# Kernel optimization log

Measured on AMD Instinct MI355X. Metric: run time of the kernel, lower is better.

## Reference

```python
import jax, jax.numpy as jnp
import numpy as np

# dims
B, NN, D, HD, L, H, S, FIN = 2048, 64, 128, 128, 4, 8, 8, 16
N = B * NN              # total nodes = 131072
EPG = 8 * NN            # edges per graph (avg degree 8)
E = B * EPG             # total edges = 1048576
A = S * (S - 1)         # num_actions per head = 56


def setup_inputs() -> dict:
    key = jax.random.key(0)
    ks = jax.random.split(key, 16)
    def nrm(k, shape, scale=0.05):
        return jax.random.normal(k, shape, jnp.float32) * scale
    x = jax.random.normal(ks[0], (N, FIN), jnp.float32)
    # per-graph random edges (src/dst local in [0, NN), offset by graph id)
    off = jnp.repeat(jnp.arange(B, dtype=jnp.int32) * NN, EPG)
    src = jax.random.randint(ks[1], (E,), 0, NN, jnp.int32) + off
    dst = jax.random.randint(ks[2], (E,), 0, NN, jnp.int32) + off
    edge_index = jnp.stack([src, dst])
    batch = (jnp.arange(N, dtype=jnp.int32) // NN)
    subsets = jnp.arange(H * S, dtype=jnp.int32).reshape(H, S)
    return dict(
        x=x, edge_index=edge_index, batch=batch, subsets=subsets,
        W_in=nrm(ks[3], (FIN, D)), b_in=jnp.zeros(D, jnp.float32),
        W_self=nrm(ks[4], (L, D, D)), W_nbr=nrm(ks[5], (L, D, D)),
        b_enc=jnp.zeros((L, D), jnp.float32),
        ext_W=nrm(ks[6], (H, 2 * D, HD)), ext_b=jnp.zeros((H, HD), jnp.float32),
        ln_g=jnp.ones((H, HD), jnp.float32), ln_b=jnp.zeros((H, HD), jnp.float32),
        hub_W=nrm(ks[7], (HD, HD)), hub_b=jnp.zeros(HD, jnp.float32),
        pol_W1=nrm(ks[8], (H, 2 * HD, HD)), pol_b1=jnp.zeros((H, HD), jnp.float32),
        pol_W2=nrm(ks[9], (H, HD, A)), pol_b2=jnp.zeros((H, A), jnp.float32),
        val_W1=nrm(ks[10], (D, D)), val_b1=jnp.zeros(D, jnp.float32),
        val_W2=nrm(ks[11], (D, 1)), val_b2=jnp.zeros(1, jnp.float32),
    )


def _forward(floats, edge_index, batch, subsets):
    (x, W_in, b_in, W_self, W_nbr, b_enc, ext_W, ext_b, ln_g, ln_b,
     hub_W, hub_b, pol_W1, pol_b1, pol_W2, pol_b2,
     val_W1, val_b1, val_W2, val_b2) = floats
    src, dst = edge_index[0], edge_index[1]
    # --- GraphEncoder: input proj + L layers of mean-aggregate message passing ---
    deg = jnp.maximum(
        jax.ops.segment_sum(jnp.ones(src.shape[0], x.dtype), dst, num_segments=N), 1.0
    )[:, None]
    h = jax.nn.relu(x @ W_in + b_in)                      # [N, D]
    for l in range(L):
        agg = jax.ops.segment_sum(h[src], dst, num_segments=N) / deg
        h = jax.nn.relu(h @ W_self[l] + agg @ W_nbr[l] + b_enc[l])
    # --- batched per-graph / per-head subset pooling (replaces python loop) ---
    he = h.reshape(B, NN, D)                              # graphs are contiguous in `batch`
    sub = he[:, subsets]                                  # [B, H, S, D]
    pooled = jnp.concatenate([sub.mean(2), sub.max(2)], axis=-1)   # [B, H, 2D]
    z = jnp.einsum('bhf,hfd->bhd', pooled, ext_W) + ext_b
    mu = z.mean(-1, keepdims=True)
    var = z.var(-1, keepdims=True)
    head_emb = jax.nn.relu((z - mu) / jnp.sqrt(var + 1e-5) * ln_g + ln_b)  # [B, H, HD]
    # --- CommunicationHub: shared global context from mean over heads ---
    ctx = jax.nn.relu(head_emb.mean(1) @ hub_W + hub_b)   # [B, HD]
    # --- PolicyHeads: per-head MLP on concat(head_emb, context) ---
    pc = jnp.concatenate(
        [head_emb, jnp.broadcast_to(ctx[:, None, :], head_emb.shape)], axis=-1)
    hh = jax.nn.relu(jnp.einsum('bhf,hfd->bhd', pc, pol_W1) + pol_b1)
    logits = jnp.einsum('bhd,hda->bha', hh, pol_W2) + pol_b2       # [B, H, A]
    # --- ValueHead: per-graph mean pool -> MLP -> tanh ---
    gm = he.mean(1)                                        # segment mean (equal-size graphs)
    v = jnp.tanh(jax.nn.relu(gm @ val_W1 + val_b1) @ val_W2 + val_b2)  # [B, 1]
    return logits, v


def reference(x, edge_index, batch, subsets, W_in, b_in, W_self, W_nbr, b_enc,
              ext_W, ext_b, ln_g, ln_b, hub_W, hub_b, pol_W1, pol_b1, pol_W2,
              pol_b2, val_W1, val_b1, val_W2, val_b2):
    floats = (x, W_in, b_in, W_self, W_nbr, b_enc, ext_W, ext_b, ln_g, ln_b,
              hub_W, hub_b, pol_W1, pol_b1, pol_W2, pol_b2,
              val_W1, val_b1, val_W2, val_b2)
    return _forward(floats, edge_index, batch, subsets)
```

## Files before the change

kernel.cpp:

```cpp
#include <hip/hip_runtime.h>

#define E_TOT 1048576
#define LOGITS 917504

typedef short bf16x8 __attribute__((ext_vector_type(8)));
typedef float f32x4 __attribute__((ext_vector_type(4)));
typedef unsigned short u16;
typedef unsigned int u32;

#define DEV static __device__ __forceinline__

DEV u16 f2bf(float f){ u32 u = __float_as_uint(f); return (u16)((u + 0x7fffu + ((u>>16)&1u))>>16); }
DEV u32 pack2(float a, float b){ return (u32)f2bf(a) | ((u32)f2bf(b)<<16); }
DEV float bf2f(u16 h){ return __uint_as_float(((u32)h)<<16); }
DEV void unpack8(uint4 u, float* f){
  f[0]=__uint_as_float(u.x<<16); f[1]=__uint_as_float(u.x&0xffff0000u);
  f[2]=__uint_as_float(u.y<<16); f[3]=__uint_as_float(u.y&0xffff0000u);
  f[4]=__uint_as_float(u.z<<16); f[5]=__uint_as_float(u.z&0xffff0000u);
  f[6]=__uint_as_float(u.w<<16); f[7]=__uint_as_float(u.w&0xffff0000u);
}
DEV uint4 pack8(const float* f){
  uint4 u; u.x=pack2(f[0],f[1]); u.y=pack2(f[2],f[3]); u.z=pack2(f[4],f[5]); u.w=pack2(f[6],f[7]); return u;
}

#define GNN_E   0
#define EXT_E   131072
#define POL1_E  393216
#define POL2_E  655360
#define HUB_E   720896
#define VW1T_E  737280
#define POOL_E  753664
#define CTX_E   4947968

__global__ __launch_bounds__(256) void pack_w(
    const float* __restrict__ Wself, const float* __restrict__ Wnbr,
    const float* __restrict__ extW,  const float* __restrict__ polW1,
    const float* __restrict__ polW2, const float* __restrict__ hubW,
    const float* __restrict__ valW1, const float* __restrict__ W_in,
    u16* __restrict__ ws)
{
  int idx = (blockIdx.x*256 + threadIdx.x)<<3;
  float v[8];
  if (idx < 131072){
    int l = idx>>15, r = idx&32767;
    int m = (r>>14)&1, r2 = r&16383;
    int kb=(r2>>12)&3, ct=(r2>>9)&7, lane=(r2>>3)&63;
    int k0 = kb*32 + ((lane>>4)<<3), n = (ct<<4)+(lane&15);
    const float* W = m? Wnbr : Wself;
    #pragma unroll
    for (int j=0;j<8;j++) v[j]=W[(l<<14)+((k0+j)<<7)+n];
    *(uint4*)&ws[GNN_E+idx]=pack8(v);
  } else if (idx < 655360){
    int i = idx - 131072;
    int isPol = (i >= 262144); if (isPol) i -= 262144;
    int h = i>>15, r = i&32767;
    int kb=(r>>12)&7, ct=(r>>9)&7, lane=(r>>3)&63;
    int k0 = kb*32 + ((lane>>4)<<3), n = (ct<<4)+(lane&15);
    const float* W = isPol? polW1 : extW;
    #pragma unroll
    for (int j=0;j<8;j++) v[j]=W[(h<<15)+((k0+j)<<7)+n];
    *(uint4*)&ws[(isPol?POL1_E:EXT_E)+i]=pack8(v);
  } else if (idx < 720896){
    int i = idx - 655360;
    int h = i>>13, r = i&8191;
    int kb=(r>>11)&3, ct=(r>>9)&3, lane=(r>>3)&63;
    int k0=kb*32+((lane>>4)<<3), n=(ct<<4)+(lane&15);
    #pragma unroll
    for (int j=0;j<8;j++) v[j]=(n<56)? polW2[h*7168+(k0+j)*56+n] : 0.0f;
    *(uint4*)&ws[POL2_E+i]=pack8(v);
  } else if (idx < 737280){
    int i = idx-720896;
    int kb=(i>>12)&3, ct=(i>>9)&7, lane=(i>>3)&63;
    int k0=kb*32+((lane>>4)<<3), n=(ct<<4)+(lane&15);
    #pragma unroll
    for (int j=0;j<8;j++) v[j]=hubW[((k0+j)<<7)+n];
    *(uint4*)&ws[HUB_E+i]=pack8(v);
  } else if (idx < 753664){
    int i = idx-737280;
    int c = i>>7, k0 = i&127;
    #pragma unroll
    for (int j=0;j<8;j++) v[j]=valW1[((k0+j)<<7)+c];
    *(uint4*)&ws[VW1T_E+i]=pack8(v);
  } else if (idx < 757760){
    int i = idx-753664;
    int ct=(i>>9)&7, lane=(i>>3)&63;
    int k0=((lane>>4)<<3), n=(ct<<4)+(lane&15);
    #pragma unroll
    for (int j=0;j<8;j++) v[j]=(k0+j<16)? W_in[((k0+j)<<7)+n] : 0.0f;
    *(uint4*)&ws[CTX_E+i]=pack8(v);
  }
}

DEV void epi_write(u16* h_bf, u16* ht, f32x4 (&acc)[4][2], float b0, float b1,
                   int wv, int r15, int kh)
{
  float bias[2] = {b0, b1};
  #pragma unroll
  for (int rt=0;rt<4;rt++){
    int sch = (rt<<1)+(kh>>1);
    int r0  = (rt<<4)+(kh<<2);
    #pragma unroll
    for (int cc=0;cc<2;cc++){
      int col=(wv<<5)+(cc<<4)+r15;
      float v0=fmaxf(acc[rt][cc][0]+bias[cc],0.0f);
      float v1=fmaxf(acc[rt][cc][1]+bias[cc],0.0f);
      float v2=fmaxf(acc[rt][cc][2]+bias[cc],0.0f);
      float v3=fmaxf(acc[rt][cc][3]+bias[cc],0.0f);
      int chc=(col>>3);
      h_bf[((r0+0)<<7)+(((chc^((r0+0)&7))<<3)|(col&7))]=f2bf(v0);
      h_bf[((r0+1)<<7)+(((chc^((r0+1)&7))<<3)|(col&7))]=f2bf(v1);
      h_bf[((r0+2)<<7)+(((chc^((r0+2)&7))<<3)|(col&7))]=f2bf(v2);
      h_bf[((r0+3)<<7)+(((chc^((r0+3)&7))<<3)|(col&7))]=f2bf(v3);
      uint2 w; w.x=pack2(v0,v1); w.y=pack2(v2,v3);
      *(uint2*)&ht[(col<<6)+(((sch^(col&7))<<3)|((kh&1)<<2))]=w;
    }
  }
}

__global__ __launch_bounds__(256,3) void gnn_kernel(
  const float* __restrict__ x, const int* __restrict__ ei,
  const int* __restrict__ subsets, const float* __restrict__ b_in,
  const float* __restrict__ b_enc, const float* __restrict__ val_b1,
  const float* __restrict__ val_W2, const float* __restrict__ val_b2,
  const u16* __restrict__ packGNN, const u16* __restrict__ packWIN,
  const u16* __restrict__ valW1T,
  u16* __restrict__ pooled, float* __restrict__ out)
{
  __shared__ __align__(16) u16 h_bf[8192];
  __shared__ __align__(16) u16 ht[8192];
  __shared__ __align__(16) u16 agg_bf[8192];
  __shared__ float deg_inv[64];
  __shared__ int subs_s[64];
  __shared__ float gmbuf[128];
  __shared__ float redbuf[4];

  int t=threadIdx.x, b=blockIdx.x;
  int lane=t&63, wv=t>>6, r15=lane&15, kh=lane>>4, ctb=wv<<1;
  u32* cnt=(u32*)ht;
  f32x4 zero4={0.0f,0.0f,0.0f,0.0f};

  int e0=(b<<9)+(t<<1);
  int2 sp=*(const int2*)&ei[e0];
  int2 dp=*(const int2*)&ei[E_TOT+e0];
  int s0=sp.x&63, s1=sp.y&63, d0=dp.x&63, d1=dp.y&63;
  if (t<64) subs_s[t]=subsets[t];
  for (int i=t;i<1024;i+=256) ((uint4*)cnt)[i]=make_uint4(0,0,0,0);
  __syncthreads();
  atomicAdd(&cnt[(d0<<6)+((((s0>>3)^(d0&7))<<3)|(s0&7))],1u);
  atomicAdd(&cnt[(d1<<6)+((((s1>>3)^(d1&7))<<3)|(s1&7))],1u);
  __syncthreads();
  if (t<64){
    u32 s=0;
    for (int k2=0;k2<16;k2++){ uint4 vv=((uint4*)cnt)[(t<<4)+k2]; s+=vv.x+vv.y+vv.z+vv.w; }
    deg_inv[t]=1.0f/(float)(s>0u?s:1u);
  }
  __syncthreads();

  bf16x8 adjf[4][2];
  #pragma unroll
  for (int ct=0;ct<4;ct++){
    int dst=(ct<<4)+r15; float di=deg_inv[dst];
    #pragma unroll
    for (int kb=0;kb<2;kb++){
      int cb=(kb<<2)+kh;
      const u32* p=&cnt[(dst<<6)+((cb^(dst&7))<<3)];
      uint4 lo=*(const uint4*)p, hi=*(const uint4*)(p+4);
      uint4 pk;
      pk.x=pack2((float)lo.x*di,(float)lo.y*di);
      pk.y=pack2((float)lo.z*di,(float)lo.w*di);
      pk.z=pack2((float)hi.x*di,(float)hi.y*di);
      pk.w=pack2((float)hi.z*di,(float)hi.w*di);
      adjf[ct][kb]=*(bf16x8*)&pk;
    }
  }

  u16* xb=agg_bf;
  { int row=t>>2, c0=(t&3)<<3;
    float v[8];
    if (c0<16){
      const float* xg=x+(b<<10)+(row<<4)+c0;
      #pragma unroll
      for (int j=0;j<8;j++) v[j]=xg[j];
    } else {
      #pragma unroll
      for (int j=0;j<8;j++) v[j]=0.0f;
    }
    *(uint4*)&xb[(row<<5)+((((c0>>3)^(row&3))<<3))]=pack8(v);
  }
  __syncthreads();

  {
    bf16x8 bw0=*(const bf16x8*)&packWIN[(ctb<<9)+(lane<<3)];
    bf16x8 bw1=*(const bf16x8*)&packWIN[((ctb+1)<<9)+(lane<<3)];
    f32x4 acc[4][2];
    #pragma unroll
    for (int rt=0;rt<4;rt++){ acc[rt][0]=zero4; acc[rt][1]=zero4; }
    #pragma unroll
    for (int rt=0;rt<4;rt++){
      int row=(rt<<4)+r15;
      bf16x8 af=*(const bf16x8*)&xb[(row<<5)+((kh^(row&3))<<3)];
      acc[rt][0]=__builtin_amdgcn_mfma_f32_16x16x32_bf16(af,bw0,acc[rt][0],0,0,0);
      acc[rt][1]=__builtin_amdgcn_mfma_f32_16x16x32_bf16(af,bw1,acc[rt][1],0,0,0);
    }
    float bi0=b_in[(wv<<5)+r15], bi1=b_in[(wv<<5)+16+r15];
    epi_write(h_bf,ht,acc,bi0,bi1,wv,r15,kh);
  }
  __syncthreads();

  #pragma unroll 1
  for (int l=0;l<4;l++){
    const u16* pl = packGNN + (l<<15);
    f32x4 a2[2][4];
    #pragma unroll
    for (int rt=0;rt<2;rt++){ a2[rt][0]=zero4; a2[rt][1]=zero4; a2[rt][2]=zero4; a2[rt][3]=zero4; }
    #pragma unroll
    for (int kb=0;kb<2;kb++){
      #pragma unroll
      for (int rt=0;rt<2;rt++){
        int dim=((ctb+rt)<<4)+r15;
        bf16x8 af=*(const bf16x8*)&ht[(dim<<6)+((((kb<<2)+kh)^(dim&7))<<3)];
        #pragma unroll
        for (int ct=0;ct<4;ct++)
          a2[rt][ct]=__builtin_amdgcn_mfma_f32_16x16x32_bf16(af,adjf[ct][kb],a2[rt][ct],0,0,0);
      }
    }
    #pragma unroll
    for (int rt=0;rt<2;rt++){
      int dch=((ctb+rt)<<1)+(kh>>1);
      #pragma unroll
      for (int ct=0;ct<4;ct++){
        int node=(ct<<4)+r15;
        uint2 w; w.x=pack2(a2[rt][ct][0],a2[rt][ct][1]); w.y=pack2(a2[rt][ct][2],a2[rt][ct][3]);
        *(uint2*)&agg_bf[(node<<7)+(((dch^(node&7))<<3)|((kh&1)<<2))]=w;
      }
    }
    __syncthreads();
    f32x4 acc[4][2];
    #pragma unroll
    for (int rt=0;rt<4;rt++){ acc[rt][0]=zero4; acc[rt][1]=zero4; }
    #pragma unroll 2
    for (int kb=0;kb<4;kb++){
      int ch=(kb<<2)+kh;
      bf16x8 bs0=*(const bf16x8*)&pl[(kb<<12)+(ctb<<9)+(lane<<3)];
      bf16x8 bs1=*(const bf16x8*)&pl[(kb<<12)+((ctb+1)<<9)+(lane<<3)];
      bf16x8 bn0=*(const bf16x8*)&pl[16384+(kb<<12)+(ctb<<9)+(lane<<3)];
      bf16x8 bn1=*(const bf16x8*)&pl[16384+(kb<<12)+((ctb+1)<<9)+(lane<<3)];
      #pragma unroll
      for (int rt=0;rt<4;rt++){
        int row=(rt<<4)+r15;
        bf16x8 af=*(const bf16x8*)&h_bf[(row<<7)+((ch^(row&7))<<3)];
        acc[rt][0]=__builtin_amdgcn_mfma_f32_16x16x32_bf16(af,bs0,acc[rt][0],0,0,0);
        acc[rt][1]=__builtin_amdgcn_mfma_f32_16x16x32_bf16(af,bs1,acc[rt][1],0,0,0);
      }
      #pragma unroll
      for (int rt=0;rt<4;rt++){
        int row=(rt<<4)+r15;
        bf16x8 ag=*(const bf16x8*)&agg_bf[(row<<7)+((ch^(row&7))<<3)];
        acc[rt][0]=__builtin_amdgcn_mfma_f32_16x16x32_bf16(ag,bn0,acc[rt][0],0,0,0);
        acc[rt][1]=__builtin_amdgcn_mfma_f32_16x16x32_bf16(ag,bn1,acc[rt][1],0,0,0);
      }
    }
    float be0=b_enc[(l<<7)+(wv<<5)+r15], be1=b_enc[(l<<7)+(wv<<5)+16+r15];
    __syncthreads();
    epi_write(h_bf,ht,acc,be0,be1,wv,r15,kh);
    __syncthreads();
  }

  {
    int hd=t>>5, q=t&31, cb=q<<2;
    float ms[4]={0,0,0,0}, mx[4]={-3e38f,-3e38f,-3e38f,-3e38f};
    int ch=cb>>3;
    #pragma unroll
    for (int s=0;s<8;s++){
      int row=subs_s[(hd<<3)+s]; int sw=row&7;
      uint2 u=*(const uint2*)&h_bf[(row<<7)+(((ch^sw)<<3)|(cb&7))];
      float f0=__uint_as_float(u.x<<16), f1=__uint_as_float(u.x&0xffff0000u);
      float f2=__uint_as_float(u.y<<16), f3=__uint_as_float(u.y&0xffff0000u);
      ms[0]+=f0; ms[1]+=f1; ms[2]+=f2; ms[3]+=f3;
      mx[0]=fmaxf(mx[0],f0); mx[1]=fmaxf(mx[1],f1);
      mx[2]=fmaxf(mx[2],f2); mx[3]=fmaxf(mx[3],f3);
    }
    int base=(((b<<3)+hd)<<8);
    uint2 um,ux;
    um.x=pack2(ms[0]*0.125f,ms[1]*0.125f); um.y=pack2(ms[2]*0.125f,ms[3]*0.125f);
    ux.x=pack2(mx[0],mx[1]);               ux.y=pack2(mx[2],mx[3]);
    *(uint2*)&pooled[base+cb]    =um;
    *(uint2*)&pooled[base+128+cb]=ux;
  }

  float gsum=0.0f;
  if (t<128){
    #pragma unroll
    for (int c=0;c<8;c++){
      uint4 u=*(const uint4*)&ht[(t<<6)+(c<<3)];
      float f[8]; unpack8(u,f);
      gsum+=f[0]+f[1]+f[2]+f[3]+f[4]+f[5]+f[6]+f[7];
    }
  }
  __syncthreads();
  if (t<128) gmbuf[t]=gsum*0.015625f;
  __syncthreads();
  if (t<128){
    float acc=val_b1[t];
    const uint4* wr=(const uint4*)&valW1T[t<<7];
    #pragma unroll
    for (int c=0;c<16;c++){
      uint4 u=wr[c]; float f[8]; unpack8(u,f);
      const float* gp=&gmbuf[c<<3];
      #pragma unroll
      for (int j=0;j<8;j++) acc=fmaf(gp[j],f[j],acc);
    }
    float contrib=fmaxf(acc,0.0f)*val_W2[t];
    #pragma unroll
    for (int d=1;d<64;d<<=1) contrib+=__shfl_xor(contrib,d);
    if (lane==0) redbuf[wv]=contrib;
  }
  __syncthreads();
  if (t==0) out[LOGITS+b]=tanhf(redbuf[0]+redbuf[1]+val_b2[0]);
}

__global__ __launch_bounds__(256) void head1_kernel(
  u16* __restrict__ pooled, const u16* __restrict__ packExt,
  const float* __restrict__ ext_b, const float* __restrict__ ln_g,
  const float* __restrict__ ln_b)
{
  __shared__ __align__(16) u16 A_lds[4096];
  __shared__ float zf[16*132];
  int t=threadIdx.x, gb=blockIdx.x, hd=blockIdx.y;
  int lane=t&63, wv=t>>6, r15=lane&15, kh=lane>>4, ctb=wv<<1;
  for (int i=t;i<512;i+=256){
    int row=i>>5, ch=i&31;
    uint4 u=*(const uint4*)&pooled[(((((gb<<4)+row)<<3)+hd)<<8)+(ch<<3)];
    *(uint4*)&A_lds[(row<<8)+((ch^(row&7))<<3)]=u;
  }
  __syncthreads();
  const u16* pw=packExt+(hd<<15);
  bf16x8 bw[8][2];
  #pragma unroll
  for (int kb=0;kb<8;kb++){
    bw[kb][0]=*(const bf16x8*)&pw[(kb<<12)+(ctb<<9)+(lane<<3)];
    bw[kb][1]=*(const bf16x8*)&pw[(kb<<12)+((ctb+1)<<9)+(lane<<3)];
  }
  f32x4 zero4={0.0f,0.0f,0.0f,0.0f};
  f32x4 acc[2]={zero4,zero4};
  #pragma unroll
  for (int kb=0;kb<8;kb++){
    int ch=(kb<<2)+kh;
    bf16x8 a=*(const bf16x8*)&A_lds[(r15<<8)+((ch^(r15&7))<<3)];
    acc[0]=__builtin_amdgcn_mfma_f32_16x16x32_bf16(a,bw[kb][0],acc[0],0,0,0);
    acc[1]=__builtin_amdgcn_mfma_f32_16x16x32_bf16(a,bw[kb][1],acc[1],0,0,0);
  }
  float eb[2]={ext_b[(hd<<7)+(wv<<5)+r15], ext_b[(hd<<7)+(wv<<5)+16+r15]};
  #pragma unroll
  for (int cc=0;cc<2;cc++){
    int col=(wv<<5)+(cc<<4)+r15;
    #pragma unroll
    for (int i=0;i<4;i++) zf[((kh<<2)+i)*132+col]=acc[cc][i]+eb[cc];
  }
  __syncthreads();
  int row=t>>4, q=t&15;
  const float* zr=&zf[row*132+(q<<3)];
  float s=0,ss=0;
  #pragma unroll
  for (int i=0;i<8;i++){ float v=zr[i]; s+=v; ss+=v*v; }
  s+=__shfl_xor(s,1); ss+=__shfl_xor(ss,1);
  s+=__shfl_xor(s,2); ss+=__shfl_xor(ss,2);
  s+=__shfl_xor(s,4); ss+=__shfl_xor(ss,4);
  s+=__shfl_xor(s,8); ss+=__shfl_xor(ss,8);
  float mu=s*0.0078125f, var=ss*0.0078125f-mu*mu, rstd=rsqrtf(var+1e-5f);
  const float* g=&ln_g[(hd<<7)+(q<<3)];
  const float* bb=&ln_b[(hd<<7)+(q<<3)];
  float e[8];
  #pragma unroll
  for (int i=0;i<8;i++) e[i]=fmaxf((zr[i]-mu)*rstd*g[i]+bb[i],0.0f);
  *(uint4*)&pooled[(((((gb<<4)+row)<<3)+hd)<<8)+(q<<3)]=pack8(e);
}

__global__ __launch_bounds__(256) void ctx_kernel(
  const u16* __restrict__ pooled, const u16* __restrict__ packHub,
  const float* __restrict__ hub_b, u16* __restrict__ ctx)
{
  __shared__ __align__(16) u16 m_lds[2048];
  int t=threadIdx.x, gb=blockIdx.x;
  int lane=t&63, wv=t>>6, r15=lane&15, kh=lane>>4, ctb=wv<<1;
  {
    int row=t>>4, ch=t&15;
    float a8[8]={0,0,0,0,0,0,0,0};
    #pragma unroll
    for (int h=0;h<8;h++){
      uint4 u=*(const uint4*)&pooled[(((((gb<<4)+row)<<3)+h)<<8)+(ch<<3)];
      float f[8]; unpack8(u,f);
      #pragma unroll
      for (int k=0;k<8;k++) a8[k]+=f[k];
    }
    #pragma unroll
    for (int k=0;k<8;k++) a8[k]*=0.125f;
    *(uint4*)&m_lds[(row<<7)+((ch^(row&7))<<3)]=pack8(a8);
  }
  __syncthreads();
  bf16x8 bh[4][2];
  #pragma unroll
  for (int kb=0;kb<4;kb++){
    bh[kb][0]=*(const bf16x8*)&packHub[(kb<<12)+(ctb<<9)+(lane<<3)];
    bh[kb][1]=*(const bf16x8*)&packHub[(kb<<12)+((ctb+1)<<9)+(lane<<3)];
  }
  f32x4 zero4={0.0f,0.0f,0.0f,0.0f};
  f32x4 acc[2]={zero4,zero4};
  #pragma unroll
  for (int kb=0;kb<4;kb++){
    int ch=(kb<<2)+kh;
    bf16x8 a=*(const bf16x8*)&m_lds[(r15<<7)+((ch^(r15&7))<<3)];
    acc[0]=__builtin_amdgcn_mfma_f32_16x16x32_bf16(a,bh[kb][0],acc[0],0,0,0);
    acc[1]=__builtin_amdgcn_mfma_f32_16x16x32_bf16(a,bh[kb][1],acc[1],0,0,0);
  }
  float hb[2]={hub_b[(wv<<5)+r15], hub_b[(wv<<5)+16+r15]};
  #pragma unroll
  for (int cc=0;cc<2;cc++){
    int col=(wv<<5)+(cc<<4)+r15;
    #pragma unroll
    for (int i=0;i<4;i++){
      int row=(kh<<2)+i;
      ctx[(((gb<<4)+row)<<7)+col]=f2bf(fmaxf(acc[cc][i]+hb[cc],0.0f));
    }
  }
}

__global__ __launch_bounds__(256) void pol_kernel(
  const u16* __restrict__ pooled, const u16* __restrict__ ctx,
  const u16* __restrict__ packPol1, const u16* __restrict__ packPol2,
  const float* __restrict__ pol_b1, const float* __restrict__ pol_b2,
  float* __restrict__ out)
{
  __shared__ __align__(16) u16 A_lds[4096];
  __shared__ __align__(16) u16 hh[2048];
  int t=threadIdx.x, gb=blockIdx.x, hd=blockIdx.y;
  int lane=t&63, wv=t>>6, r15=lane&15, kh=lane>>4, ctb=wv<<1;
  for (int i=t;i<512;i+=256){
    int row=i>>5, ch=i&31;
    uint4 u;
    if (ch<16) u=*(const uint4*)&pooled[(((((gb<<4)+row)<<3)+hd)<<8)+(ch<<3)];
    else       u=*(const uint4*)&ctx[(((gb<<4)+row)<<7)+((ch-16)<<3)];
    *(uint4*)&A_lds[(row<<8)+((ch^(row&7))<<3)]=u;
  }
  __syncthreads();
  const u16* pw=packPol1+(hd<<15);
  bf16x8 bw[8][2];
  #pragma unroll
  for (int kb=0;kb<8;kb++){
    bw[kb][0]=*(const bf16x8*)&pw[(kb<<12)+(ctb<<9)+(lane<<3)];
    bw[kb][1]=*(const bf16x8*)&pw[(kb<<12)+((ctb+1)<<9)+(lane<<3)];
  }
  f32x4 zero4={0.0f,0.0f,0.0f,0.0f};
  f32x4 acc[2]={zero4,zero4};
  #pragma unroll
  for (int kb=0;kb<8;kb++){
    int ch=(kb<<2)+kh;
    bf16x8 a=*(const bf16x8*)&A_lds[(r15<<8)+((ch^(r15&7))<<3)];
    acc[0]=__builtin_amdgcn_mfma_f32_16x16x32_bf16(a,bw[kb][0],acc[0],0,0,0);
    acc[1]=__builtin_amdgcn_mfma_f32_16x16x32_bf16(a,bw[kb][1],acc[1],0,0,0);
  }
  float pb[2]={pol_b1[(hd<<7)+(wv<<5)+r15], pol_b1[(hd<<7)+(wv<<5)+16+r15]};
  #pragma unroll
  for (int cc=0;cc<2;cc++){
    int col=(wv<<5)+(cc<<4)+r15;
    #pragma unroll
    for (int i=0;i<4;i++){
      int row=(kh<<2)+i;
      float v=fmaxf(acc[cc][i]+pb[cc],0.0f);
      hh[(row<<7)+((((col>>3)^(row&7))<<3)|(col&7))]=f2bf(v);
    }
  }
  __syncthreads();
  const u16* p2=packPol2+(hd<<13);
  bf16x8 b2[4];
  #pragma unroll
  for (int kb=0;kb<4;kb++)
    b2[kb]=*(const bf16x8*)&p2[(kb<<11)+(wv<<9)+(lane<<3)];
  f32x4 a2=zero4;
  #pragma unroll
  for (int kb=0;kb<4;kb++){
    int ch=(kb<<2)+kh;
    bf16x8 a=*(const bf16x8*)&hh[(r15<<7)+((ch^(r15&7))<<3)];
    a2=__builtin_amdgcn_mfma_f32_16x16x32_bf16(a,b2[kb],a2,0,0,0);
  }
  int col=(wv<<4)+r15;
  if (col<56){
    float pb2=pol_b2[hd*56+col];
    #pragma unroll
    for (int i=0;i<4;i++){
      int row=(kh<<2)+i;
      out[(((((gb<<4)+row)<<3)+hd)*56)+col]=a2[i]+pb2;
    }
  }
}

extern "C" void kernel_launch(void* const* d_in, const int* in_sizes, int n_in,
                              void* d_out, int out_size, void* d_ws, size_t ws_size,
                              hipStream_t stream)
{
  const float* x     =(const float*)d_in[0];
  const int*   ei    =(const int*)  d_in[1];
  const int*   subs  =(const int*)  d_in[3];
  const float* W_in  =(const float*)d_in[4];
  const float* b_in  =(const float*)d_in[5];
  const float* W_self=(const float*)d_in[6];
  const float* W_nbr =(const float*)d_in[7];
  const float* b_enc =(const float*)d_in[8];
  const float* extW  =(const float*)d_in[9];
  const float* ext_b =(const float*)d_in[10];
  const float* ln_g  =(const float*)d_in[11];
  const float* ln_b  =(const float*)d_in[12];
  const float* hubW  =(const float*)d_in[13];
  const float* hub_b =(const float*)d_in[14];
  const float* polW1 =(const float*)d_in[15];
  const float* pol_b1=(const float*)d_in[16];
  const float* polW2 =(const float*)d_in[17];
  const float* pol_b2=(const float*)d_in[18];
  const float* valW1 =(const float*)d_in[19];
  const float* val_b1=(const float*)d_in[20];
  const float* valW2 =(const float*)d_in[21];
  const float* val_b2=(const float*)d_in[22];
  float* out=(float*)d_out;
  u16* ws=(u16*)d_ws;

  pack_w<<<370,256,0,stream>>>(W_self,W_nbr,extW,polW1,polW2,hubW,valW1,W_in,ws);
  gnn_kernel<<<2048,256,0,stream>>>(x,ei,subs,b_in,b_enc,val_b1,valW2,val_b2,
      ws+GNN_E, ws+CTX_E, ws+VW1T_E, ws+POOL_E, out);
  head1_kernel<<<dim3(128,8),256,0,stream>>>(ws+POOL_E, ws+EXT_E, ext_b, ln_g, ln_b);
  ctx_kernel<<<128,256,0,stream>>>(ws+POOL_E, ws+HUB_E, hub_b, ws+CTX_E);
  pol_kernel<<<dim3(128,8),256,0,stream>>>(ws+POOL_E, ws+CTX_E, ws+POL1_E, ws+POL2_E,
      pol_b1, pol_b2, out);
}
```

Baseline: 192.3 us.

## Fuse extractor, hub and policy head kernels into one per-graph-block kernel

Merges the three head kernels (extractor+LayerNorm, communication hub, policy MLP) into a single kernel where each block handles 8 graphs and loops over all 8 heads. Intermediate head embeddings and context stay in LDS instead of round-tripping through global memory, and two kernel launches are dropped. The cost is a smaller grid (256 blocks instead of 1024) and half-empty MFMA tiles, since only 8 of 16 rows are valid. Head loops are also serialized, with extra barriers per head.

```diff
diff --git a/kernel.cpp b/kernel.cpp
--- a/kernel.cpp
+++ b/kernel.cpp
@@ -319,76 +319,80 @@
   if (t==0) out[LOGITS+b]=tanhf(redbuf[0]+redbuf[1]+val_b2[0]);
 }
 
-__global__ __launch_bounds__(256) void head1_kernel(
-  u16* __restrict__ pooled, const u16* __restrict__ packExt,
+__global__ __launch_bounds__(256) void heads_kernel(
+  const u16* __restrict__ pooled, const u16* __restrict__ packExt,
   const float* __restrict__ ext_b, const float* __restrict__ ln_g,
-  const float* __restrict__ ln_b)
+  const float* __restrict__ ln_b, const u16* __restrict__ packHub,
+  const float* __restrict__ hub_b, const u16* __restrict__ packPol1,
+  const u16* __restrict__ packPol2, const float* __restrict__ pol_b1,
+  const float* __restrict__ pol_b2, float* __restrict__ out)
 {
-  __shared__ __align__(16) u16 A_lds[4096];
-  __shared__ float zf[16*132];
-  int t=threadIdx.x, gb=blockIdx.x, hd=blockIdx.y;
-  int lane=t&63, wv=t>>6, r15=lane&15, kh=lane>>4, ctb=wv<<1;
-  for (int i=t;i<512;i+=256){
-    int row=i>>5, ch=i&31;
-    uint4 u=*(const uint4*)&pooled[(((((gb<<4)+row)<<3)+hd)<<8)+(ch<<3)];
-    *(uint4*)&A_lds[(row<<8)+((ch^(row&7))<<3)]=u;
-  }
-  __syncthreads();
-  const u16* pw=packExt+(hd<<15);
-  bf16x8 bw[8][2];
-  #pragma unroll
-  for (int kb=0;kb<8;kb++){
-    bw[kb][0]=*(const bf16x8*)&pw[(kb<<12)+(ctb<<9)+(lane<<3)];
-    bw[kb][1]=*(const bf16x8*)&pw[(kb<<12)+((ctb+1)<<9)+(lane<<3)];
-  }
-  f32x4 zero4={0.0f,0.0f,0.0f,0.0f};
-  f32x4 acc[2]={zero4,zero4};
-  #pragma unroll
-  for (int kb=0;kb<8;kb++){
-    int ch=(kb<<2)+kh;
-    bf16x8 a=*(const bf16x8*)&A_lds[(r15<<8)+((ch^(r15&7))<<3)];
-    acc[0]=__builtin_amdgcn_mfma_f32_16x16x32_bf16(a,bw[kb][0],acc[0],0,0,0);
-    acc[1]=__builtin_amdgcn_mfma_f32_16x16x32_bf16(a,bw[kb][1],acc[1],0,0,0);
-  }
-  float eb[2]={ext_b[(hd<<7)+(wv<<5)+r15], ext_b[(hd<<7)+(wv<<5)+16+r15]};
-  #pragma unroll
-  for (int cc=0;cc<2;cc++){
-    int col=(wv<<5)+(cc<<4)+r15;
-    #pragma unroll
-    for (int i=0;i<4;i++) zf[((kh<<2)+i)*132+col]=acc[cc][i]+eb[cc];
-  }
-  __syncthreads();
-  int row=t>>4, q=t&15;
-  const float* zr=&zf[row*132+(q<<3)];
-  float s=0,ss=0;
-  #pragma unroll
-  for (int i=0;i<8;i++){ float v=zr[i]; s+=v; ss+=v*v; }
-  s+=__shfl_xor(s,1); ss+=__shfl_xor(ss,1);
-  s+=__shfl_xor(s,2); ss+=__shfl_xor(ss,2);
-  s+=__shfl_xor(s,4); ss+=__shfl_xor(ss,4);
-  s+=__shfl_xor(s,8); ss+=__shfl_xor(ss,8);
-  float mu=s*0.0078125f, var=ss*0.0078125f-mu*mu, rstd=rsqrtf(var+1e-5f);
-  const float* g=&ln_g[(hd<<7)+(q<<3)];
-  const float* bb=&ln_b[(hd<<7)+(q<<3)];
-  float e[8];
-  #pragma unroll
-  for (int i=0;i<8;i++) e[i]=fmaxf((zr[i]-mu)*rstd*g[i]+bb[i],0.0f);
-  *(uint4*)&pooled[(((((gb<<4)+row)<<3)+hd)<<8)+(q<<3)]=pack8(e);
-}
-
-__global__ __launch_bounds__(256) void ctx_kernel(
-  const u16* __restrict__ pooled, const u16* __restrict__ packHub,
-  const float* __restrict__ hub_b, u16* __restrict__ ctx)
-{
-  __shared__ __align__(16) u16 m_lds[2048];
+  __shared__ __align__(16) u16 A_lds[2048];
+  __shared__ float zf[8*132];
+  __shared__ __align__(16) u16 he[8192];
+  __shared__ __align__(16) u16 ctx_l[1024];
+  __shared__ __align__(16) u16 m_lds[1024];
+  __shared__ __align__(16) u16 hh[1024];
   int t=threadIdx.x, gb=blockIdx.x;
   int lane=t&63, wv=t>>6, r15=lane&15, kh=lane>>4, ctb=wv<<1;
-  {
+  int ar=r15&7;
+  f32x4 zero4={0.0f,0.0f,0.0f,0.0f};
+
+  for (int hd=0; hd<8; ++hd){
+    { int row=t>>5, ch=t&31;
+      uint4 u=*(const uint4*)&pooled[(((((gb<<3)+row)<<3)+hd)<<8)+(ch<<3)];
+      *(uint4*)&A_lds[(row<<8)+((ch^(row&7))<<3)]=u;
+    }
+    __syncthreads();
+    const u16* pw=packExt+(hd<<15);
+    f32x4 acc[2]={zero4,zero4};
+    #pragma unroll
+    for (int kb=0;kb<8;kb++){
+      int ch=(kb<<2)+kh;
+      bf16x8 a=*(const bf16x8*)&A_lds[(ar<<8)+((ch^ar)<<3)];
+      bf16x8 b0=*(const bf16x8*)&pw[(kb<<12)+(ctb<<9)+(lane<<3)];
+      bf16x8 b1=*(const bf16x8*)&pw[(kb<<12)+((ctb+1)<<9)+(lane<<3)];
+      acc[0]=__builtin_amdgcn_mfma_f32_16x16x32_bf16(a,b0,acc[0],0,0,0);
+      acc[1]=__builtin_amdgcn_mfma_f32_16x16x32_bf16(a,b1,acc[1],0,0,0);
+    }
+    if (kh<2){
+      float eb[2]={ext_b[(hd<<7)+(wv<<5)+r15], ext_b[(hd<<7)+(wv<<5)+16+r15]};
+      #pragma unroll
+      for (int cc=0;cc<2;cc++){
+        int col=(wv<<5)+(cc<<4)+r15;
+        #pragma unroll
+        for (int i=0;i<4;i++) zf[((kh<<2)+i)*132+col]=acc[cc][i]+eb[cc];
+      }
+    }
+    __syncthreads();
+    if (t<128){
+      int row=t>>4, q=t&15;
+      const float* zr=&zf[row*132+(q<<3)];
+      float s=0,ss=0;
+      #pragma unroll
+      for (int i=0;i<8;i++){ float v=zr[i]; s+=v; ss+=v*v; }
+      s+=__shfl_xor(s,1); ss+=__shfl_xor(ss,1);
+      s+=__shfl_xor(s,2); ss+=__shfl_xor(ss,2);
+      s+=__shfl_xor(s,4); ss+=__shfl_xor(ss,4);
+      s+=__shfl_xor(s,8); ss+=__shfl_xor(ss,8);
+      float mu=s*0.0078125f, var=ss*0.0078125f-mu*mu, rstd=rsqrtf(var+1e-5f);
+      const float* g=&ln_g[(hd<<7)+(q<<3)];
+      const float* bb=&ln_b[(hd<<7)+(q<<3)];
+      float e[8];
+      #pragma unroll
+      for (int i=0;i<8;i++) e[i]=fmaxf((zr[i]-mu)*rstd*g[i]+bb[i],0.0f);
+      int r=(row<<3)+hd;
+      *(uint4*)&he[(r<<7)+((q^hd)<<3)]=pack8(e);
+    }
+    __syncthreads();
+  }
+
+  if (t<128){
     int row=t>>4, ch=t&15;
     float a8[8]={0,0,0,0,0,0,0,0};
     #pragma unroll
     for (int h=0;h<8;h++){
-      uint4 u=*(const uint4*)&pooled[(((((gb<<4)+row)<<3)+h)<<8)+(ch<<3)];
+      uint4 u=*(const uint4*)&he[(((row<<3)+h)<<7)+((ch^h)<<3)];
       float f[8]; unpack8(u,f);
       #pragma unroll
       for (int k=0;k<8;k++) a8[k]+=f[k];
@@ -398,99 +402,84 @@
     *(uint4*)&m_lds[(row<<7)+((ch^(row&7))<<3)]=pack8(a8);
   }
   __syncthreads();
-  bf16x8 bh[4][2];
-  #pragma unroll
-  for (int kb=0;kb<4;kb++){
-    bh[kb][0]=*(const bf16x8*)&packHub[(kb<<12)+(ctb<<9)+(lane<<3)];
-    bh[kb][1]=*(const bf16x8*)&packHub[(kb<<12)+((ctb+1)<<9)+(lane<<3)];
-  }
-  f32x4 zero4={0.0f,0.0f,0.0f,0.0f};
-  f32x4 acc[2]={zero4,zero4};
-  #pragma unroll
-  for (int kb=0;kb<4;kb++){
-    int ch=(kb<<2)+kh;
-    bf16x8 a=*(const bf16x8*)&m_lds[(r15<<7)+((ch^(r15&7))<<3)];
-    acc[0]=__builtin_amdgcn_mfma_f32_16x16x32_bf16(a,bh[kb][0],acc[0],0,0,0);
-    acc[1]=__builtin_amdgcn_mfma_f32_16x16x32_bf16(a,bh[kb][1],acc[1],0,0,0);
-  }
-  float hb[2]={hub_b[(wv<<5)+r15], hub_b[(wv<<5)+16+r15]};
-  #pragma unroll
-  for (int cc=0;cc<2;cc++){
-    int col=(wv<<5)+(cc<<4)+r15;
-    #pragma unroll
-    for (int i=0;i<4;i++){
-      int row=(kh<<2)+i;
-      ctx[(((gb<<4)+row)<<7)+col]=f2bf(fmaxf(acc[cc][i]+hb[cc],0.0f));
-    }
-  }
-}
-
-__global__ __launch_bounds__(256) void pol_kernel(
-  const u16* __restrict__ pooled, const u16* __restrict__ ctx,
-  const u16* __restrict__ packPol1, const u16* __restrict__ packPol2,
-  const float* __restrict__ pol_b1, const float* __restrict__ pol_b2,
-  float* __restrict__ out)
-{
-  __shared__ __align__(16) u16 A_lds[4096];
-  __shared__ __align__(16) u16 hh[2048];
-  int t=threadIdx.x, gb=blockIdx.x, hd=blockIdx.y;
-  int lane=t&63, wv=t>>6, r15=lane&15, kh=lane>>4, ctb=wv<<1;
-  for (int i=t;i<512;i+=256){
-    int row=i>>5, ch=i&31;
-    uint4 u;
-    if (ch<16) u=*(const uint4*)&pooled[(((((gb<<4)+row)<<3)+hd)<<8)+(ch<<3)];
-    else       u=*(const uint4*)&ctx[(((gb<<4)+row)<<7)+((ch-16)<<3)];
-    *(uint4*)&A_lds[(row<<8)+((ch^(row&7))<<3)]=u;
-  }
-  __syncthreads();
-  const u16* pw=packPol1+(hd<<15);
-  bf16x8 bw[8][2];
-  #pragma unroll
-  for (int kb=0;kb<8;kb++){
-    bw[kb][0]=*(const bf16x8*)&pw[(kb<<12)+(ctb<<9)+(lane<<3)];
-    bw[kb][1]=*(const bf16x8*)&pw[(kb<<12)+((ctb+1)<<9)+(lane<<3)];
-  }
-  f32x4 zero4={0.0f,0.0f,0.0f,0.0f};
-  f32x4 acc[2]={zero4,zero4};
-  #pragma unroll
-  for (int kb=0;kb<8;kb++){
-    int ch=(kb<<2)+kh;
-    bf16x8 a=*(const bf16x8*)&A_lds[(r15<<8)+((ch^(r15&7))<<3)];
-    acc[0]=__builtin_amdgcn_mfma_f32_16x16x32_bf16(a,bw[kb][0],acc[0],0,0,0);
-    acc[1]=__builtin_amdgcn_mfma_f32_16x16x32_bf16(a,bw[kb][1],acc[1],0,0,0);
-  }
-  float pb[2]={pol_b1[(hd<<7)+(wv<<5)+r15], pol_b1[(hd<<7)+(wv<<5)+16+r15]};
-  #pragma unroll
-  for (int cc=0;cc<2;cc++){
-    int col=(wv<<5)+(cc<<4)+r15;
-    #pragma unroll
-    for (int i=0;i<4;i++){
-      int row=(kh<<2)+i;
-      float v=fmaxf(acc[cc][i]+pb[cc],0.0f);
-      hh[(row<<7)+((((col>>3)^(row&7))<<3)|(col&7))]=f2bf(v);
-    }
-  }
-  __syncthreads();
-  const u16* p2=packPol2+(hd<<13);
-  bf16x8 b2[4];
-  #pragma unroll
-  for (int kb=0;kb<4;kb++)
-    b2[kb]=*(const bf16x8*)&p2[(kb<<11)+(wv<<9)+(lane<<3)];
-  f32x4 a2=zero4;
-  #pragma unroll
-  for (int kb=0;kb<4;kb++){
-    int ch=(kb<<2)+kh;
-    bf16x8 a=*(const bf16x8*)&hh[(r15<<7)+((ch^(r15&7))<<3)];
-    a2=__builtin_amdgcn_mfma_f32_16x16x32_bf16(a,b2[kb],a2,0,0,0);
-  }
-  int col=(wv<<4)+r15;
-  if (col<56){
-    float pb2=pol_b2[hd*56+col];
-    #pragma unroll
-    for (int i=0;i<4;i++){
-      int row=(kh<<2)+i;
-      out[(((((gb<<4)+row)<<3)+hd)*56)+col]=a2[i]+pb2;
-    }
+  {
+    f32x4 acc[2]={zero4,zero4};
+    #pragma unroll
+    for (int kb=0;kb<4;kb++){
+      int ch=(kb<<2)+kh;
+      bf16x8 a=*(const bf16x8*)&m_lds[(ar<<7)+((ch^ar)<<3)];
+      bf16x8 b0=*(const bf16x8*)&packHub[(kb<<12)+(ctb<<9)+(lane<<3)];
+      bf16x8 b1=*(const bf16x8*)&packHub[(kb<<12)+((ctb+1)<<9)+(lane<<3)];
+      acc[0]=__builtin_amdgcn_mfma_f32_16x16x32_bf16(a,b0,acc[0],0,0,0);
+      acc[1]=__builtin_amdgcn_mfma_f32_16x16x32_bf16(a,b1,acc[1],0,0,0);
+    }
+    if (kh<2){
+      float hb[2]={hub_b[(wv<<5)+r15], hub_b[(wv<<5)+16+r15]};
+      #pragma unroll
+      for (int cc=0;cc<2;cc++){
+        int col=(wv<<5)+(cc<<4)+r15;
+        #pragma unroll
+        for (int i=0;i<4;i++){
+          int row=(kh<<2)+i;
+          ctx_l[(row<<7)+((((col>>3)^(row&7))<<3)|(col&7))]=f2bf(fmaxf(acc[cc][i]+hb[cc],0.0f));
+        }
+      }
+    }
+  }
+  __syncthreads();
+
+  for (int hd=0; hd<8; ++hd){
+    { int row=t>>5, ch=t&31;
+      uint4 u;
+      if (ch<16){ int r=(row<<3)+hd; u=*(const uint4*)&he[(r<<7)+((ch^hd)<<3)]; }
+      else        u=*(const uint4*)&ctx_l[(row<<7)+(((ch-16)^(row&7))<<3)];
+      *(uint4*)&A_lds[(row<<8)+((ch^(row&7))<<3)]=u;
+    }
+    __syncthreads();
+    const u16* pw=packPol1+(hd<<15);
+    f32x4 acc[2]={zero4,zero4};
+    #pragma unroll
+    for (int kb=0;kb<8;kb++){
+      int ch=(kb<<2)+kh;
+      bf16x8 a=*(const bf16x8*)&A_lds[(ar<<8)+((ch^ar)<<3)];
+      bf16x8 b0=*(const bf16x8*)&pw[(kb<<12)+(ctb<<9)+(lane<<3)];
+      bf16x8 b1=*(const bf16x8*)&pw[(kb<<12)+((ctb+1)<<9)+(lane<<3)];
+      acc[0]=__builtin_amdgcn_mfma_f32_16x16x32_bf16(a,b0,acc[0],0,0,0);
+      acc[1]=__builtin_amdgcn_mfma_f32_16x16x32_bf16(a,b1,acc[1],0,0,0);
+    }
+    if (kh<2){
+      float pb[2]={pol_b1[(hd<<7)+(wv<<5)+r15], pol_b1[(hd<<7)+(wv<<5)+16+r15]};
+      #pragma unroll
+      for (int cc=0;cc<2;cc++){
+        int col=(wv<<5)+(cc<<4)+r15;
+        #pragma unroll
+        for (int i=0;i<4;i++){
+          int row=(kh<<2)+i;
+          float v=fmaxf(acc[cc][i]+pb[cc],0.0f);
+          hh[(row<<7)+((((col>>3)^(row&7))<<3)|(col&7))]=f2bf(v);
+        }
+      }
+    }
+    __syncthreads();
+    const u16* p2=packPol2+(hd<<13);
+    f32x4 a2=zero4;
+    #pragma unroll
+    for (int kb=0;kb<4;kb++){
+      int ch=(kb<<2)+kh;
+      bf16x8 a=*(const bf16x8*)&hh[(ar<<7)+((ch^ar)<<3)];
+      bf16x8 b2=*(const bf16x8*)&p2[(kb<<11)+(wv<<9)+(lane<<3)];
+      a2=__builtin_amdgcn_mfma_f32_16x16x32_bf16(a,b2,a2,0,0,0);
+    }
+    int col=(wv<<4)+r15;
+    if (col<56 && kh<2){
+      float pb2=pol_b2[hd*56+col];
+      #pragma unroll
+      for (int i=0;i<4;i++){
+        int row=(kh<<2)+i;
+        out[(((((gb<<3)+row)<<3)+hd)*56)+col]=a2[i]+pb2;
+      }
+    }
+    __syncthreads();
   }
 }
 
@@ -526,8 +515,6 @@
   pack_w<<<370,256,0,stream>>>(W_self,W_nbr,extW,polW1,polW2,hubW,valW1,W_in,ws);
   gnn_kernel<<<2048,256,0,stream>>>(x,ei,subs,b_in,b_enc,val_b1,valW2,val_b2,
       ws+GNN_E, ws+CTX_E, ws+VW1T_E, ws+POOL_E, out);
-  head1_kernel<<<dim3(128,8),256,0,stream>>>(ws+POOL_E, ws+EXT_E, ext_b, ln_g, ln_b);
-  ctx_kernel<<<128,256,0,stream>>>(ws+POOL_E, ws+HUB_E, hub_b, ws+CTX_E);
-  pol_kernel<<<dim3(128,8),256,0,stream>>>(ws+POOL_E, ws+CTX_E, ws+POL1_E, ws+POL2_E,
-      pol_b1, pol_b2, out);
-}
+  heads_kernel<<<256,256,0,stream>>>(ws+POOL_E, ws+EXT_E, ext_b, ln_g, ln_b,
+      ws+HUB_E, hub_b, ws+POL1_E, ws+POL2_E, pol_b1, pol_b2, out);
+}
```

After: 217.4 us. 13.0% more time.
